# Kernel optimization log

Hardware: AMD Instinct MI355X
Metric: run time of the kernel (lower is better)

## Reference

```python
import jax, jax.numpy as jnp
import numpy as np

HIDDEN = 1024

def setup_inputs() -> dict:
    key = jax.random.key(0)
    k1, k2, k3 = jax.random.split(key, 3)
    X = jax.random.normal(k1, (4, 4096, HIDDEN), dtype=jnp.float32)
    # nn.Linear(hidden, 3*hidden): weight [3h, h], bias [3h]
    W = jax.random.normal(k2, (3 * HIDDEN, HIDDEN), dtype=jnp.float32) / np.sqrt(HIDDEN)
    b = jax.random.normal(k3, (3 * HIDDEN,), dtype=jnp.float32) * 0.01
    return {"X": X, "W": W, "b": b}

def reference(X, W, b):
    h = X.shape[-1]
    QKV = jnp.einsum('bsh,oh->bso', X, W) + b  # [B,S,3h]
    Q, K, V = jnp.split(QKV, 3, axis=-1)
    scores = jnp.einsum('bqh,bkh->bqk', Q, K) / jnp.sqrt(jnp.float32(h))
    attn = jax.nn.softmax(scores, axis=-1)
    return jnp.einsum('bqk,bkh->bqh', attn, V)
```

## Files before the change

### kernel.cpp

```cpp
#include <hip/hip_runtime.h>
#include <hip/hip_bf16.h>

typedef unsigned short u16;
typedef _Float16 f16x8 __attribute__((ext_vector_type(8)));
typedef float f32x4 __attribute__((ext_vector_type(4)));

#if __has_builtin(__builtin_amdgcn_exp2f)
#define EXP2F(x) __builtin_amdgcn_exp2f(x)
#else
#define EXP2F(x) exp2f(x)
#endif
#define FA_C32 0.045084220027780106f

__device__ __forceinline__ f32x4 mfma16h(f16x8 a, f16x8 b, f32x4 c) {
  return __builtin_amdgcn_mfma_f32_16x16x32_f16(a, b, c, 0, 0, 0);
}
__device__ __forceinline__ unsigned pk2h(float a, float b) {
  union { _Float16 h[2]; unsigned u; } x;
  x.h[0] = (_Float16)a; x.h[1] = (_Float16)b;
  return x.u;
}
__device__ __forceinline__ u16 h1(float a) {
  union { _Float16 h; u16 u; } x; x.h = (_Float16)a; return x.u;
}

typedef __attribute__((address_space(1))) const unsigned int gas_u32;
typedef __attribute__((address_space(3))) unsigned int las_u32;
__device__ __forceinline__ void gl_lds16(const u16* g, u16* l) {
  __builtin_amdgcn_global_load_lds((gas_u32*)g, (las_u32*)l, 16, 0, 0);
}

__global__ __launch_bounds__(256) void cast_f16_k(const float* __restrict__ src,
                                                  u16* __restrict__ dst, int n8) {
  int i = blockIdx.x * 256 + threadIdx.x;
  if (i >= n8) return;
  const float4* s4 = (const float4*)src;
  float4 a = s4[i * 2], b = s4[i * 2 + 1];
  uint4 o;
  o.x = pk2h(a.x, a.y); o.y = pk2h(a.z, a.w);
  o.z = pk2h(b.x, b.y); o.w = pk2h(b.z, b.w);
  ((uint4*)dst)[i] = o;
}

__global__ __launch_bounds__(256) void reduce_l_k(const float* __restrict__ partial,
                                                  float* __restrict__ linv, int nrows) {
  int i = blockIdx.x * 256 + threadIdx.x;
  if (i >= nrows) return;
  const int z = i >> 12, row = i & 4095;
  const float* p = partial + (size_t)z * 16 * 4096 + row;
  float s = 0.f;
#pragma unroll
  for (int by = 0; by < 16; ++by) s += p[(size_t)by * 4096];
  linv[i] = 1.0f / s;
}

template <int K_, int EPI>
__global__ __launch_bounds__(512, 2) void gemm8p(
    const u16* __restrict__ A, const u16* __restrict__ B,
    const float* __restrict__ bias, u16* __restrict__ D0, u16* __restrict__ D1,
    u16* __restrict__ D2, float* __restrict__ Df, const int ldc,
    const size_t strA, const size_t strB, const size_t strC,
    float* __restrict__ Pr, const float* __restrict__ Lv) {
  constexpr int NT = K_ / 64;
  static_assert(NT >= 4 && (NT % 2) == 0, "need even NT >= 4");
  __shared__ __align__(16) u16 As[2][2][128 * 64];
  __shared__ __align__(16) u16 Bs[2][2][128 * 64];

  const int tid = threadIdx.x, lane = tid & 63, wid = tid >> 6;
  const int l15 = lane & 15, lhi = lane >> 4;
  const int m0 = blockIdx.x * 256, n0 = blockIdx.y * 256;
  const int wm = wid >> 2, wn = wid & 3;
  const u16* Ag = A + (size_t)blockIdx.z * strA;
  const u16* Bg = B + (size_t)blockIdx.z * strB;

  const int srow8 = lane >> 3;
  const int sblk = (lane & 7) ^ srow8;

#define STAGE_Q(BUF, G, GROW0, ST)                                        \
  gl_lds16((G) + (size_t)((GROW0) + wid * 8 + srow8) * K_ +               \
               (ST) * 64 + sblk * 8,                                      \
           (BUF) + (wid * 8) * 64)

#define BAR()                                                             \
  asm volatile("" ::: "memory");                                          \
  __builtin_amdgcn_s_barrier();                                           \
  asm volatile("" ::: "memory")

#define LGKM0()                                                           \
  asm volatile("s_waitcnt lgkmcnt(0)" ::: "memory");                      \
  __builtin_amdgcn_sched_barrier(0)

#define SB0() __builtin_amdgcn_sched_barrier(0)
#define VMC8() asm volatile("s_waitcnt vmcnt(8)" ::: "memory")
#define VMC0() asm volatile("s_waitcnt vmcnt(0)" ::: "memory")

#define RD_A(DST, PB, MH)                                                 \
  _Pragma("unroll") for (int mf = 0; mf < 4; ++mf)                        \
  _Pragma("unroll") for (int ks = 0; ks < 2; ++ks)                        \
    DST[mf][ks] = *(const f16x8*)((PB) + ((MH) * 64 + mf * 16 + l15) * 64 \
                                  + (((ks * 4 + lhi) ^ (l15 & 7)) * 8));

#define RD_B(DST, PB, BO, NH)                                             \
  _Pragma("unroll") for (int nf = 0; nf < 2; ++nf)                        \
  _Pragma("unroll") for (int ks = 0; ks < 2; ++ks)                        \
    DST[nf][ks] = *(const f16x8*)((PB) + ((BO) + (NH) * 32 + nf * 16 + l15) * 64 \
                                  + (((ks * 4 + lhi) ^ (l15 & 7)) * 8));

#define MM(AV, BV, MB, NB2)                                               \
  __builtin_amdgcn_s_setprio(1);                                          \
  _Pragma("unroll") for (int mf = 0; mf < 4; ++mf)                        \
  _Pragma("unroll") for (int nf = 0; nf < 2; ++nf)                        \
  _Pragma("unroll") for (int ks = 0; ks < 2; ++ks)                        \
    acc[(MB) * 4 + mf][(NB2) * 2 + nf] =                                  \
        mfma16h(AV[mf][ks], BV[nf][ks], acc[(MB) * 4 + mf][(NB2) * 2 + nf]); \
  __builtin_amdgcn_s_setprio(0);

  f32x4 acc[8][4];
#pragma unroll
  for (int i = 0; i < 8; ++i)
#pragma unroll
    for (int j = 0; j < 4; ++j) acc[i][j] = 0.f;

  const int bofs = (wn & 1) * 64;

#define STAGE_TILE(DB, T)                                                 \
  STAGE_Q(&As[DB][0][0],    Ag, m0,       T);                             \
  STAGE_Q(&As[DB][0][4096], Ag, m0 + 64,  T);                             \
  STAGE_Q(&As[DB][1][0],    Ag, m0 + 128, T);                             \
  STAGE_Q(&As[DB][1][4096], Ag, m0 + 192, T);                             \
  STAGE_Q(&Bs[DB][0][0],    Bg, n0,       T);                             \
  STAGE_Q(&Bs[DB][0][4096], Bg, n0 + 64,  T);                             \
  STAGE_Q(&Bs[DB][1][0],    Bg, n0 + 128, T);                             \
  STAGE_Q(&Bs[DB][1][4096], Bg, n0 + 192, T)

  STAGE_TILE(0, 0);
  STAGE_TILE(1, 1);
  VMC8();
  BAR();

#define PHASES4(DB, TN, PRE)                                              \
  {                                                                       \
    const u16* Apb = &As[DB][wm][0];                                      \
    const u16* Bpb = &Bs[DB][wn >> 1][0];                                 \
                                             \
    RD_A(a0, Apb, 0);                                                     \
    RD_B(b0, Bpb, bofs, 0);                                               \
    BAR();                                                                \
    LGKM0();                                                              \
    MM(a0, b0, 0, 0);                                                     \
    SB0();                                                                \
    BAR();                                                                \
       \
    RD_B(b1, Bpb, bofs, 1);                                               \
    if (PRE) { STAGE_Q(&As[DB][0][0], Ag, m0,       TN);                  \
               STAGE_Q(&As[DB][1][0], Ag, m0 + 128, TN); }                \
    BAR();                                                                \
    LGKM0();                                                              \
    MM(a0, b1, 0, 1);                                                     \
    SB0();                                                                \
    BAR();                                                                \
     \
    RD_A(a1, Apb, 1);                                                     \
    if (PRE) { STAGE_Q(&Bs[DB][0][0],    Bg, n0,       TN);               \
               STAGE_Q(&Bs[DB][0][4096], Bg, n0 + 64,  TN);               \
               STAGE_Q(&Bs[DB][1][0],    Bg, n0 + 128, TN);               \
               STAGE_Q(&Bs[DB][1][4096], Bg, n0 + 192, TN); }             \
    BAR();                                                                \
    LGKM0();                                                              \
    MM(a1, b1, 1, 1);                                                     \
    SB0();                                                                \
    BAR();                                                                \
     \
    if (PRE) { STAGE_Q(&As[DB][0][4096], Ag, m0 + 64,  TN);               \
               STAGE_Q(&As[DB][1][4096], Ag, m0 + 192, TN); }             \
    BAR();                                                                \
    LGKM0();                                                              \
    MM(a1, b0, 1, 0);                                                     \
    SB0();                                                                \
    if (PRE) { VMC8(); } else { VMC0(); }                                 \
    BAR();                                                                \
  }

  for (int it = 0; it < NT / 2; ++it) {
    const int t0 = 2 * it;
    const bool pre = (t0 + 2 < NT);
    f16x8 a0[4][2], a1[4][2], b0[2][2], b1[2][2];
    PHASES4(0, t0 + 2, pre)
    PHASES4(1, t0 + 3, pre)
  }
#undef PHASES4
#undef STAGE_TILE
#undef STAGE_Q
#undef BAR
#undef LGKM0
#undef SB0
#undef VMC8
#undef VMC0
#undef RD_A
#undef RD_B
#undef MM

  if (EPI == 2) {
    float bv[4];
#pragma unroll
    for (int cf = 0; cf < 4; ++cf) bv[cf] = bias[n0 + wn * 64 + cf * 16 + l15];
    const int region = n0 >> 10;
    const int ncol0 = (n0 & 1023) + wn * 64;
    if (region < 2) {
      u16* dst = region ? D1 : D0;
#pragma unroll
      for (int rf = 0; rf < 8; ++rf) {
        const int m = m0 + wm * 128 + rf * 16 + lhi * 4;
#pragma unroll
        for (int r = 0; r < 4; ++r)
#pragma unroll
          for (int cf = 0; cf < 4; ++cf)
            dst[(size_t)(m + r) * 1024 + ncol0 + cf * 16 + l15] = h1(acc[rf][cf][r] + bv[cf]);
      }
    } else {
#pragma unroll
      for (int rf = 0; rf < 8; ++rf) {
        const int m = m0 + wm * 128 + rf * 16 + lhi * 4;
        const int bb = m >> 12, s = m & 4095;
#pragma unroll
        for (int cf = 0; cf < 4; ++cf) {
          const int dcol = ncol0 + cf * 16 + l15;
          uint2 v;
          v.x = pk2h(acc[rf][cf][0] + bv[cf], acc[rf][cf][1] + bv[cf]);
          v.y = pk2h(acc[rf][cf][2] + bv[cf], acc[rf][cf][3] + bv[cf]);
          *(uint2*)&D2[(size_t)(bb * 1024 + dcol) * 4096 + s] = v;
        }
      }
    }
  } else if (EPI == 0) {
    float* rsum = (float*)&As[0][0][0];
#pragma unroll
    for (int rf = 0; rf < 8; ++rf)
#pragma unroll
      for (int r = 0; r < 4; ++r) {
        float s = 0.f;
#pragma unroll
        for (int cf = 0; cf < 4; ++cf) {
          float p = EXP2F(acc[rf][cf][r] * FA_C32);
          p = fminf(p, 60000.f);
          acc[rf][cf][r] = p;
          s += p;
        }
        s += __shfl_xor(s, 1, 64);
        s += __shfl_xor(s, 2, 64);
        s += __shfl_xor(s, 4, 64);
        s += __shfl_xor(s, 8, 64);
        if (l15 == 0) rsum[wn * 256 + wm * 128 + rf * 16 + lhi * 4 + r] = s;
      }
#pragma unroll
    for (int rf = 0; rf < 8; ++rf) {
      const int m = m0 + wm * 128 + rf * 16 + lhi * 4;
#pragma unroll
      for (int r = 0; r < 4; ++r)
#pragma unroll
        for (int cf = 0; cf < 4; ++cf) {
          const int n = n0 + wn * 64 + cf * 16 + l15;
          D0[(size_t)blockIdx.z * strC + (size_t)(m + r) * ldc + n] = h1(acc[rf][cf][r]);
        }
    }
    __syncthreads();
    if (tid < 256) {
      const float s = rsum[tid] + rsum[256 + tid] + rsum[512 + tid] + rsum[768 + tid];
      Pr[((size_t)blockIdx.z * 16 + blockIdx.y) * 4096 + m0 + tid] = s;
    }
  } else {
#pragma unroll
    for (int rf = 0; rf < 8; ++rf) {
      const int m = m0 + wm * 128 + rf * 16 + lhi * 4;
#pragma unroll
      for (int r = 0; r < 4; ++r) {
        const float li = Lv[(size_t)blockIdx.z * 4096 + m + r];
#pragma unroll
        for (int cf = 0; cf < 4; ++cf) {
          const int n = n0 + wn * 64 + cf * 16 + l15;
          Df[(size_t)blockIdx.z * strC + (size_t)(m + r) * ldc + n] = acc[rf][cf][r] * li;
        }
      }
    }
  }
}

extern "C" void kernel_launch(void* const* d_in, const int* in_sizes, int n_in,
                              void* d_out, int out_size, void* d_ws, size_t ws_size,
                              hipStream_t stream) {
  const float* X = (const float*)d_in[0];
  const float* W = (const float*)d_in[1];
  const float* b = (const float*)d_in[2];
  float* out = (float*)d_out;
  char* ws = (char*)d_ws;

  const size_t SB = (size_t)4096 * 4096 * 2;
  const size_t QB = (size_t)4096 * 1024 * 2;
  const size_t WFB = (size_t)3072 * 1024 * 2;
  int NB = 1;
  if (ws_size >= 4 * SB + WFB + 12 * QB) NB = 4;
  else if (ws_size >= 2 * SB + WFB + 12 * QB) NB = 2;

  u16* S  = (u16*)(ws);
  u16* Xf = (u16*)(ws);
  u16* Wf = (u16*)(ws + (size_t)NB * SB);
  u16* Qf = (u16*)(ws + (size_t)NB * SB + WFB);
  u16* Kf = (u16*)(ws + (size_t)NB * SB + WFB + 4 * QB);
  u16* Vt = (u16*)(ws + (size_t)NB * SB + WFB + 8 * QB);
  float* Pr = (float*)Wf;
  float* Lv = Pr + (size_t)NB * 16 * 4096;

  cast_f16_k<<<8192, 256, 0, stream>>>(X, Xf, 16777216 / 8);
  cast_f16_k<<<1536, 256, 0, stream>>>(W, Wf, 3145728 / 8);

  gemm8p<1024, 2><<<dim3(64, 12, 1), 512, 0, stream>>>(
      Xf, Wf, b, Qf, Kf, Vt, nullptr, 0, 0, 0, 0, nullptr, nullptr);

  const size_t strQ = (size_t)4096 * 1024;
  const size_t strS = (size_t)4096 * 4096;
  const size_t strV = (size_t)1024 * 4096;
  for (int g = 0; g < 4; g += NB) {
    const u16* Qg = Qf + (size_t)g * strQ;
    const u16* Kg = Kf + (size_t)g * strQ;
    const u16* Vg = Vt + (size_t)g * strV;
    float* Og = out + (size_t)g * strQ;
    gemm8p<1024, 0><<<dim3(16, 16, NB), 512, 0, stream>>>(
        Qg, Kg, nullptr, S, nullptr, nullptr, nullptr, 4096, strQ, strQ, strS,
        Pr, nullptr);
    reduce_l_k<<<NB * 16, 256, 0, stream>>>(Pr, Lv, NB * 4096);
    gemm8p<4096, 1><<<dim3(16, 4, NB), 512, 0, stream>>>(
        S, Vg, nullptr, nullptr, nullptr, nullptr, Og, 1024, strS, strV, strQ,
        nullptr, Lv);
  }
}
```

Before: 432.4 us.

## Compute softmax row sums inside PV GEMM via fdot2 over A fragments

The separate row-sum path is removed: the QK^T epilogue no longer reduces exp values or writes partial sums, and the reduce kernel is deleted. Instead the P·V GEMM accumulates row sums of the fp16 P tiles it already loads into registers, using fdot2 against ones in the wn==0 waves. It then combines them with shuffles and LDS and applies the reciprocal in the epilogue. This drops a kernel launch, the partial-sum global traffic and the epilogue shuffles. In exchange it adds extra VALU work and register pressure to the main loop of the larger GEMM, and the sums now come from fp16-rounded P values.

```diff
diff --git a/kernel.cpp b/kernel.cpp
--- a/kernel.cpp
+++ b/kernel.cpp
@@ -3,6 +3,7 @@
 
 typedef unsigned short u16;
 typedef _Float16 f16x8 __attribute__((ext_vector_type(8)));
+typedef _Float16 f16x2 __attribute__((ext_vector_type(2)));
 typedef float f32x4 __attribute__((ext_vector_type(4)));
 
 #if __has_builtin(__builtin_amdgcn_exp2f)
@@ -23,6 +24,16 @@
 __device__ __forceinline__ u16 h1(float a) {
   union { _Float16 h; u16 u; } x; x.h = (_Float16)a; return x.u;
 }
+
+#if __has_builtin(__builtin_amdgcn_fdot2)
+__device__ __forceinline__ float fdot2_(f16x2 a, f16x2 b, float c) {
+  return __builtin_amdgcn_fdot2(a, b, c, false);
+}
+#else
+__device__ __forceinline__ float fdot2_(f16x2 a, f16x2 b, float c) {
+  return c + (float)a[0] * (float)b[0] + (float)a[1] * (float)b[1];
+}
+#endif
 
 typedef __attribute__((address_space(1))) const unsigned int gas_u32;
 typedef __attribute__((address_space(3))) unsigned int las_u32;
@@ -42,29 +53,17 @@
   ((uint4*)dst)[i] = o;
 }
 
-__global__ __launch_bounds__(256) void reduce_l_k(const float* __restrict__ partial,
-                                                  float* __restrict__ linv, int nrows) {
-  int i = blockIdx.x * 256 + threadIdx.x;
-  if (i >= nrows) return;
-  const int z = i >> 12, row = i & 4095;
-  const float* p = partial + (size_t)z * 16 * 4096 + row;
-  float s = 0.f;
-#pragma unroll
-  for (int by = 0; by < 16; ++by) s += p[(size_t)by * 4096];
-  linv[i] = 1.0f / s;
-}
-
 template <int K_, int EPI>
 __global__ __launch_bounds__(512, 2) void gemm8p(
     const u16* __restrict__ A, const u16* __restrict__ B,
     const float* __restrict__ bias, u16* __restrict__ D0, u16* __restrict__ D1,
     u16* __restrict__ D2, float* __restrict__ Df, const int ldc,
-    const size_t strA, const size_t strB, const size_t strC,
-    float* __restrict__ Pr, const float* __restrict__ Lv) {
+    const size_t strA, const size_t strB, const size_t strC) {
   constexpr int NT = K_ / 64;
   static_assert(NT >= 4 && (NT % 2) == 0, "need even NT >= 4");
   __shared__ __align__(16) u16 As[2][2][128 * 64];
   __shared__ __align__(16) u16 Bs[2][2][128 * 64];
+  __shared__ float lds_l[256];
 
   const int tid = threadIdx.x, lane = tid & 63, wid = tid >> 6;
   const int l15 = lane & 15, lhi = lane >> 4;
@@ -115,11 +114,28 @@
         mfma16h(AV[mf][ks], BV[nf][ks], acc[(MB) * 4 + mf][(NB2) * 2 + nf]); \
   __builtin_amdgcn_s_setprio(0);
 
+#define SUMA(FR, MH8)                                                     \
+  if (EPI == 1 && wn == 0) {                                              \
+    _Pragma("unroll") for (int mf = 0; mf < 4; ++mf)                      \
+    _Pragma("unroll") for (int ks = 0; ks < 2; ++ks) {                    \
+      const f16x2* _pr = (const f16x2*)&FR[mf][ks];                       \
+      _Pragma("unroll") for (int j = 0; j < 4; ++j)                       \
+        lsa[MH8][mf] = fdot2_(_pr[j], ones2, lsa[MH8][mf]);               \
+    }                                                                     \
+  }
+
   f32x4 acc[8][4];
 #pragma unroll
   for (int i = 0; i < 8; ++i)
 #pragma unroll
     for (int j = 0; j < 4; ++j) acc[i][j] = 0.f;
+
+  float lsa[2][4];
+#pragma unroll
+  for (int i = 0; i < 2; ++i)
+#pragma unroll
+    for (int j = 0; j < 4; ++j) lsa[i][j] = 0.f;
+  const f16x2 ones2 = {(_Float16)1.0f, (_Float16)1.0f};
 
   const int bofs = (wn & 1) * 64;
 
@@ -148,6 +164,7 @@
     BAR();                                                                \
     LGKM0();                                                              \
     MM(a0, b0, 0, 0);                                                     \
+    SUMA(a0, 0);                                                          \
     SB0();                                                                \
     BAR();                                                                \
        \
@@ -168,6 +185,7 @@
     BAR();                                                                \
     LGKM0();                                                              \
     MM(a1, b1, 1, 1);                                                     \
+    SUMA(a1, 1);                                                          \
     SB0();                                                                \
     BAR();                                                                \
      \
@@ -199,6 +217,7 @@
 #undef RD_A
 #undef RD_B
 #undef MM
+#undef SUMA
 
   if (EPI == 2) {
     float bv[4];
@@ -233,25 +252,6 @@
       }
     }
   } else if (EPI == 0) {
-    float* rsum = (float*)&As[0][0][0];
-#pragma unroll
-    for (int rf = 0; rf < 8; ++rf)
-#pragma unroll
-      for (int r = 0; r < 4; ++r) {
-        float s = 0.f;
-#pragma unroll
-        for (int cf = 0; cf < 4; ++cf) {
-          float p = EXP2F(acc[rf][cf][r] * FA_C32);
-          p = fminf(p, 60000.f);
-          acc[rf][cf][r] = p;
-          s += p;
-        }
-        s += __shfl_xor(s, 1, 64);
-        s += __shfl_xor(s, 2, 64);
-        s += __shfl_xor(s, 4, 64);
-        s += __shfl_xor(s, 8, 64);
-        if (l15 == 0) rsum[wn * 256 + wm * 128 + rf * 16 + lhi * 4 + r] = s;
-      }
 #pragma unroll
     for (int rf = 0; rf < 8; ++rf) {
       const int m = m0 + wm * 128 + rf * 16 + lhi * 4;
@@ -260,21 +260,29 @@
 #pragma unroll
         for (int cf = 0; cf < 4; ++cf) {
           const int n = n0 + wn * 64 + cf * 16 + l15;
-          D0[(size_t)blockIdx.z * strC + (size_t)(m + r) * ldc + n] = h1(acc[rf][cf][r]);
+          float p = fminf(EXP2F(acc[rf][cf][r] * FA_C32), 60000.f);
+          D0[(size_t)blockIdx.z * strC + (size_t)(m + r) * ldc + n] = h1(p);
+        }
+    }
+  } else {
+    if (wn == 0) {
+#pragma unroll
+      for (int mh = 0; mh < 2; ++mh)
+#pragma unroll
+        for (int mf = 0; mf < 4; ++mf) {
+          float s = lsa[mh][mf];
+          s += __shfl_xor(s, 16, 64);
+          s += __shfl_xor(s, 32, 64);
+          if (lhi == 0) lds_l[wm * 128 + mh * 64 + mf * 16 + l15] = s;
         }
     }
     __syncthreads();
-    if (tid < 256) {
-      const float s = rsum[tid] + rsum[256 + tid] + rsum[512 + tid] + rsum[768 + tid];
-      Pr[((size_t)blockIdx.z * 16 + blockIdx.y) * 4096 + m0 + tid] = s;
-    }
-  } else {
 #pragma unroll
     for (int rf = 0; rf < 8; ++rf) {
       const int m = m0 + wm * 128 + rf * 16 + lhi * 4;
 #pragma unroll
       for (int r = 0; r < 4; ++r) {
-        const float li = Lv[(size_t)blockIdx.z * 4096 + m + r];
+        const float li = 1.0f / lds_l[wm * 128 + rf * 16 + lhi * 4 + r];
 #pragma unroll
         for (int cf = 0; cf < 4; ++cf) {
           const int n = n0 + wn * 64 + cf * 16 + l15;
@@ -307,14 +315,12 @@
   u16* Qf = (u16*)(ws + (size_t)NB * SB + WFB);
   u16* Kf = (u16*)(ws + (size_t)NB * SB + WFB + 4 * QB);
   u16* Vt = (u16*)(ws + (size_t)NB * SB + WFB + 8 * QB);
-  float* Pr = (float*)Wf;
-  float* Lv = Pr + (size_t)NB * 16 * 4096;
 
   cast_f16_k<<<8192, 256, 0, stream>>>(X, Xf, 16777216 / 8);
   cast_f16_k<<<1536, 256, 0, stream>>>(W, Wf, 3145728 / 8);
 
   gemm8p<1024, 2><<<dim3(64, 12, 1), 512, 0, stream>>>(
-      Xf, Wf, b, Qf, Kf, Vt, nullptr, 0, 0, 0, 0, nullptr, nullptr);
+      Xf, Wf, b, Qf, Kf, Vt, nullptr, 0, 0, 0, 0);
 
   const size_t strQ = (size_t)4096 * 1024;
   const size_t strS = (size_t)4096 * 4096;
@@ -325,11 +331,8 @@
     const u16* Vg = Vt + (size_t)g * strV;
     float* Og = out + (size_t)g * strQ;
     gemm8p<1024, 0><<<dim3(16, 16, NB), 512, 0, stream>>>(
-        Qg, Kg, nullptr, S, nullptr, nullptr, nullptr, 4096, strQ, strQ, strS,
-        Pr, nullptr);
-    reduce_l_k<<<NB * 16, 256, 0, stream>>>(Pr, Lv, NB * 4096);
+        Qg, Kg, nullptr, S, nullptr, nullptr, nullptr, 4096, strQ, strQ, strS);
     gemm8p<4096, 1><<<dim3(16, 4, NB), 512, 0, stream>>>(
-        S, Vg, nullptr, nullptr, nullptr, nullptr, Og, 1024, strS, strV, strQ,
-        nullptr, Lv);
-  }
-}
+        S, Vg, nullptr, nullptr, nullptr, nullptr, Og, 1024, strS, strV, strQ);
+  }
+}
```

After: 417.4 us. 3.5% less time.
